# Kernel tuning notes

Measured on AMD Instinct MI355X. Metric: run time of the kernel, lower is better.

## Reference

```python
import jax, jax.numpy as jnp
import numpy as np

B, PD, CD = 8192, 1024, 1024


def setup_inputs() -> dict:
    key = jax.random.key(0)
    ks = jax.random.split(key, 10)
    u = lambda k, shape: jax.random.uniform(k, shape, dtype=jnp.float32, minval=-0.05, maxval=0.05)
    return {
        "P": jax.random.normal(ks[0], (B, PD), dtype=jnp.float32),
        "C1": jax.random.normal(ks[1], (B, CD), dtype=jnp.float32),
        "C2": jax.random.normal(ks[2], (B, CD), dtype=jnp.float32),
        "C3": jax.random.normal(ks[3], (B, CD), dtype=jnp.float32),
        "C4": jax.random.normal(ks[4], (B, CD), dtype=jnp.float32),
        "GateWeight_P": u(ks[5], (PD, CD)),
        "GateWeight_C": u(ks[6], (CD, CD)),
        "GateBias": u(ks[7], (CD,)),
        "OutWeight": u(ks[8], (PD, CD)),
        "OutBias": u(ks[9], (CD, 1)),
    }


def reference(P, C1, C2, C3, C4, GateWeight_P, GateWeight_C, GateBias, OutWeight, OutBias):
    # Stack the 4 choice branches: [4, B, C]
    Cs = jnp.stack([C1, C2, C3, C4], axis=0)
    WP = P @ GateWeight_P                                  # [B, C]
    WC = jnp.einsum("kbc,cd->kbd", Cs, GateWeight_C)       # [4, B, C]
    g = jax.nn.sigmoid(WP[None] + WC + GateBias)           # [4, B, C]
    C_dash = Cs * g                                        # [4, B, C]
    WP_out = P @ OutWeight                                 # [B, C]
    scores = jnp.einsum("kbc,bc->kb", C_dash, WP_out)      # batch_dot axes=[1,1]
    bias = jnp.einsum("kbc,c->kb", C_dash, OutBias[:, 0])  # K.dot(C_dash, OutBias)
    return (scores + bias).T                               # [B, 4]
```

## Files before the change

### kernel.cpp

```cpp
#include <hip/hip_runtime.h>
#include <hip/hip_bf16.h>


#define B_  8192
#define PD_ 1024
#define CD_ 1024

typedef unsigned short ushort_t;
typedef __attribute__((ext_vector_type(8))) short    short8;
typedef __attribute__((ext_vector_type(8))) unsigned short ushort8;
typedef __attribute__((ext_vector_type(4))) float    floatx4;

__device__ __forceinline__ float bf2f(unsigned short u) {
    return __uint_as_float(((unsigned)u) << 16);
}
__device__ __forceinline__ unsigned short f2bf(float f) {
    unsigned u = __float_as_uint(f);
    unsigned r = u + 0x7FFFu + ((u >> 16) & 1u);
    return (unsigned short)(r >> 16);
}

__global__ __launch_bounds__(256) void cast5_kernel(const float* __restrict__ P,
                                                    const float* __restrict__ C1,
                                                    const float* __restrict__ C2,
                                                    const float* __restrict__ C3,
                                                    const float* __restrict__ C4,
                                                    ushort_t* __restrict__ Pb,
                                                    ushort_t* __restrict__ Call) {
    const int seg = blockIdx.x >> 13;
    const int i   = (blockIdx.x & 8191) * 256 + threadIdx.x;
    const float* src;
    ushort_t* dst;
    switch (seg) {
        case 0: src = P;  dst = Pb; break;
        case 1: src = C1; dst = Call; break;
        case 2: src = C2; dst = Call + (size_t)1 * B_ * CD_; break;
        case 3: src = C3; dst = Call + (size_t)2 * B_ * CD_; break;
        default: src = C4; dst = Call + (size_t)3 * B_ * CD_; break;
    }
    float4 v = ((const float4*)src)[i];
    ushort4 o;
    o.x = f2bf(v.x); o.y = f2bf(v.y); o.z = f2bf(v.z); o.w = f2bf(v.w);
    ((ushort4*)dst)[i] = o;
}

__global__ __launch_bounds__(256) void transpose3(const float* __restrict__ GWP,
                                                  const float* __restrict__ OW,
                                                  const float* __restrict__ GWC,
                                                  ushort_t* __restrict__ Wcat,
                                                  ushort_t* __restrict__ GWCt) {
    __shared__ float tile[32][33];
    const float* src;
    ushort_t* dst;
    switch (blockIdx.z) {
        case 0: src = GWP; dst = Wcat; break;
        case 1: src = OW;  dst = Wcat + 1024 * 1024; break;
        default: src = GWC; dst = GWCt; break;
    }
    const int R = 1024, C = 1024;
    int c0 = blockIdx.x * 32, r0 = blockIdx.y * 32;
    int x = threadIdx.x, y = threadIdx.y;
    for (int i = y; i < 32; i += 8)
        tile[i][x] = src[(size_t)(r0 + i) * C + c0 + x];
    __syncthreads();
    for (int i = y; i < 32; i += 8)
        dst[(size_t)(c0 + i) * R + r0 + x] = f2bf(tile[x][i]);
}

__device__ __forceinline__ void gl_lds16(const void* g, void* l) {
    __builtin_amdgcn_global_load_lds((const __attribute__((address_space(1))) void*)g,
                                     (__attribute__((address_space(3))) void*)l, 16, 0, 0);
}

__global__ __launch_bounds__(256) void gemm_fused(const ushort_t* __restrict__ Pb,
                                                  const ushort_t* __restrict__ Wcat,
                                                  ushort_t* __restrict__ WPcat,
                                                  const ushort_t* __restrict__ Call,
                                                  const ushort_t* __restrict__ GWCt,
                                                  ushort_t* __restrict__ WC) {
    __shared__ ushort_t lA[128 * 32];
    __shared__ ushort_t lB[128 * 32];
    const int K = 1024;

    const ushort_t *A, *Bt;
    ushort_t* Cc;
    int N, tileM, tileN;
    const int bid = blockIdx.x;
    if (bid < 1024) {
        A = Pb; Bt = Wcat; Cc = WPcat; N = 2048;
        tileN = (bid & 15) * 128; tileM = (bid >> 4) * 128;
    } else {
        const int b2 = bid - 1024;
        A = Call; Bt = GWCt; Cc = WC; N = 1024;
        tileN = (b2 & 7) * 128; tileM = (b2 >> 3) * 128;
    }

    const int t    = threadIdx.x;
    const int wave = t >> 6, lane = t & 63;
    const int quad = lane >> 4, l16 = lane & 15;
    const int wm   = wave >> 1, wn  = wave & 1;

    const int ch0  = wave * 2;
    const int srow = lane >> 2;
    const int skc  = (lane & 3) ^ ((lane >> 4) & 3);
    const int sc   = skc * 8;
    const int lo0  = ch0 * 512 + lane * 8;

    const ushort_t* Ag0 = A  + (size_t)(tileM + ch0 * 16 + srow)      * K + sc;
    const ushort_t* Ag1 = A  + (size_t)(tileM + ch0 * 16 + srow + 16) * K + sc;
    const ushort_t* Bg0 = Bt + (size_t)(tileN + ch0 * 16 + srow)      * K + sc;
    const ushort_t* Bg1 = Bt + (size_t)(tileN + ch0 * 16 + srow + 16) * K + sc;

    const int fro = (l16 * 4 + (quad ^ (l16 >> 2))) * 8;

    floatx4 acc[4][4];
#pragma unroll
    for (int i = 0; i < 4; i++)
#pragma unroll
        for (int j = 0; j < 4; j++) acc[i][j] = (floatx4)0.f;

    for (int k0 = 0; k0 < K; k0 += 32) {
        gl_lds16(Ag0 + k0, &lA[lo0]);
        gl_lds16(Ag1 + k0, &lA[lo0 + 512]);
        gl_lds16(Bg0 + k0, &lB[lo0]);
        gl_lds16(Bg1 + k0, &lB[lo0 + 512]);
        __syncthreads();

        short8 af[4], bfr[4];
#pragma unroll
        for (int mi = 0; mi < 4; mi++)
            af[mi] = *(const short8*)&lA[(wm * 4 + mi) * 512 + fro];
#pragma unroll
        for (int ni = 0; ni < 4; ni++)
            bfr[ni] = *(const short8*)&lB[(wn * 4 + ni) * 512 + fro];
#pragma unroll
        for (int mi = 0; mi < 4; mi++)
#pragma unroll
            for (int ni = 0; ni < 4; ni++)
                acc[mi][ni] = __builtin_amdgcn_mfma_f32_16x16x32_bf16(
                    af[mi], bfr[ni], acc[mi][ni], 0, 0, 0);
        __syncthreads();
    }

#pragma unroll
    for (int mi = 0; mi < 4; mi++)
#pragma unroll
        for (int ni = 0; ni < 4; ni++)
#pragma unroll
            for (int r = 0; r < 4; r++) {
                int row = tileM + wm * 64 + mi * 16 + quad * 4 + r;
                int col = tileN + wn * 64 + ni * 16 + l16;
                Cc[(size_t)row * N + col] = f2bf(acc[mi][ni][r]);
            }
}

__global__ __launch_bounds__(256) void epilogue(const ushort_t* __restrict__ WPcat,
                                                const ushort_t* __restrict__ WC,
                                                const ushort_t* __restrict__ Call,
                                                const float* __restrict__ Gb,
                                                const float* __restrict__ Ob,
                                                float* __restrict__ out) {
    const int wave = threadIdx.x >> 6, lane = threadIdx.x & 63;
    const int b = blockIdx.x * 4 + wave;
    float acc[4] = {0.f, 0.f, 0.f, 0.f};

#pragma unroll
    for (int it = 0; it < 2; it++) {
        const int c = it * 512 + lane * 8;
        ushort8 wp  = *(const ushort8*)&WPcat[(size_t)b * 2048 + c];
        ushort8 wpo = *(const ushort8*)&WPcat[(size_t)b * 2048 + 1024 + c];
        floatx4 g0 = *(const floatx4*)&Gb[c];
        floatx4 g1 = *(const floatx4*)&Gb[c + 4];
        floatx4 o0 = *(const floatx4*)&Ob[c];
        floatx4 o1 = *(const floatx4*)&Ob[c + 4];
        float gb[8], ob[8];
#pragma unroll
        for (int j = 0; j < 4; j++) { gb[j] = g0[j]; gb[4 + j] = g1[j]; ob[j] = o0[j]; ob[4 + j] = o1[j]; }

        float po[8], wpf[8];
#pragma unroll
        for (int j = 0; j < 8; j++) {
            wpf[j] = bf2f(wp[j]);
            po[j]  = bf2f(wpo[j]) + ob[j];
        }
#pragma unroll
        for (int k = 0; k < 4; k++) {
            size_t off = ((size_t)k * B_ + b) * 1024 + c;
            ushort8 cv = *(const ushort8*)&Call[off];
            ushort8 wc = *(const ushort8*)&WC[off];
            float s = 0.f;
#pragma unroll
            for (int j = 0; j < 8; j++) {
                float x = wpf[j] + bf2f(wc[j]) + gb[j];
                float g = 1.f / (1.f + __expf(-x));
                s += bf2f(cv[j]) * g * po[j];
            }
            acc[k] += s;
        }
    }
#pragma unroll
    for (int k = 0; k < 4; k++) {
#pragma unroll
        for (int off = 32; off > 0; off >>= 1)
            acc[k] += __shfl_down(acc[k], off);
    }
    if (lane == 0) {
        out[(size_t)b * 4 + 0] = acc[0];
        out[(size_t)b * 4 + 1] = acc[1];
        out[(size_t)b * 4 + 2] = acc[2];
        out[(size_t)b * 4 + 3] = acc[3];
    }
}

extern "C" void kernel_launch(void* const* d_in, const int* in_sizes, int n_in,
                              void* d_out, int out_size, void* d_ws, size_t ws_size,
                              hipStream_t stream) {
    (void)in_sizes; (void)n_in; (void)out_size; (void)ws_size;
    const float* P   = (const float*)d_in[0];
    const float* C1  = (const float*)d_in[1];
    const float* C2  = (const float*)d_in[2];
    const float* C3  = (const float*)d_in[3];
    const float* C4  = (const float*)d_in[4];
    const float* GWP = (const float*)d_in[5];
    const float* GWC = (const float*)d_in[6];
    const float* Gb  = (const float*)d_in[7];
    const float* OW  = (const float*)d_in[8];
    const float* Ob  = (const float*)d_in[9];
    float* out = (float*)d_out;

    char* ws = (char*)d_ws;
    ushort_t* Pb    = (ushort_t*)(ws);
    ushort_t* Call  = (ushort_t*)(ws + (16u  << 20));
    ushort_t* Wcat  = (ushort_t*)(ws + (80u  << 20));
    ushort_t* GWCt  = (ushort_t*)(ws + (84u  << 20));
    ushort_t* WPcat = (ushort_t*)(ws + (86u  << 20));
    ushort_t* WC    = (ushort_t*)(ws + (118u << 20));

    cast5_kernel<<<5 * 8192, 256, 0, stream>>>(P, C1, C2, C3, C4, Pb, Call);
    transpose3<<<dim3(32, 32, 3), dim3(32, 8), 0, stream>>>(GWP, OW, GWC, Wcat, GWCt);

    gemm_fused<<<3072, 256, 0, stream>>>(Pb, Wcat, WPcat, Call, GWCt, WC);

    epilogue<<<B_ / 4, 256, 0, stream>>>(WPcat, WC, Call, Gb, Ob, out);
}
```

Baseline: 361.6 us.

## Fuse gating epilogue into choice GEMM with atomic score accumulation

The gate epilogue now runs inside the WC GEMM. Each block stages its bf16 WC tile in shared memory, computes the sigmoid gate and the dot-product contributions, and atomically adds partial scores to the output. This removes the write and re-read of the 64MB WC intermediate and one kernel launch. The cast and transpose prep kernels are merged into one launch that also zeroes the output. The P GEMM is split into its own kernel, which now runs before the choice GEMM instead of concurrently, and the fused epilogue adds atomics and scattered WPcat reads.

```diff
diff --git a/kernel.cpp b/kernel.cpp
--- a/kernel.cpp
+++ b/kernel.cpp
@@ -20,51 +20,60 @@
     return (unsigned short)(r >> 16);
 }
 
-__global__ __launch_bounds__(256) void cast5_kernel(const float* __restrict__ P,
-                                                    const float* __restrict__ C1,
-                                                    const float* __restrict__ C2,
-                                                    const float* __restrict__ C3,
-                                                    const float* __restrict__ C4,
-                                                    ushort_t* __restrict__ Pb,
-                                                    ushort_t* __restrict__ Call) {
-    const int seg = blockIdx.x >> 13;
-    const int i   = (blockIdx.x & 8191) * 256 + threadIdx.x;
-    const float* src;
-    ushort_t* dst;
-    switch (seg) {
-        case 0: src = P;  dst = Pb; break;
-        case 1: src = C1; dst = Call; break;
-        case 2: src = C2; dst = Call + (size_t)1 * B_ * CD_; break;
-        case 3: src = C3; dst = Call + (size_t)2 * B_ * CD_; break;
-        default: src = C4; dst = Call + (size_t)3 * B_ * CD_; break;
-    }
-    float4 v = ((const float4*)src)[i];
-    ushort4 o;
-    o.x = f2bf(v.x); o.y = f2bf(v.y); o.z = f2bf(v.z); o.w = f2bf(v.w);
-    ((ushort4*)dst)[i] = o;
-}
-
-__global__ __launch_bounds__(256) void transpose3(const float* __restrict__ GWP,
-                                                  const float* __restrict__ OW,
-                                                  const float* __restrict__ GWC,
-                                                  ushort_t* __restrict__ Wcat,
-                                                  ushort_t* __restrict__ GWCt) {
-    __shared__ float tile[32][33];
-    const float* src;
-    ushort_t* dst;
-    switch (blockIdx.z) {
-        case 0: src = GWP; dst = Wcat; break;
-        case 1: src = OW;  dst = Wcat + 1024 * 1024; break;
-        default: src = GWC; dst = GWCt; break;
-    }
-    const int R = 1024, C = 1024;
-    int c0 = blockIdx.x * 32, r0 = blockIdx.y * 32;
-    int x = threadIdx.x, y = threadIdx.y;
-    for (int i = y; i < 32; i += 8)
-        tile[i][x] = src[(size_t)(r0 + i) * C + c0 + x];
-    __syncthreads();
-    for (int i = y; i < 32; i += 8)
-        dst[(size_t)(c0 + i) * R + r0 + x] = f2bf(tile[x][i]);
+__global__ __launch_bounds__(256) void prep_kernel(const float* __restrict__ P,
+                                                   const float* __restrict__ C1,
+                                                   const float* __restrict__ C2,
+                                                   const float* __restrict__ C3,
+                                                   const float* __restrict__ C4,
+                                                   const float* __restrict__ GWP,
+                                                   const float* __restrict__ OW,
+                                                   const float* __restrict__ GWC,
+                                                   ushort_t* __restrict__ Pb,
+                                                   ushort_t* __restrict__ Call,
+                                                   ushort_t* __restrict__ Wcat,
+                                                   ushort_t* __restrict__ GWCt,
+                                                   float* __restrict__ out) {
+    const int bid = blockIdx.x;
+    const int tid = threadIdx.x;
+    if (bid < 40960) {
+        const int seg = bid >> 13;
+        const int i   = (bid & 8191) * 256 + tid;
+        const float* src;
+        ushort_t* dst;
+        switch (seg) {
+            case 0: src = P;  dst = Pb; break;
+            case 1: src = C1; dst = Call; break;
+            case 2: src = C2; dst = Call + (size_t)1 * B_ * CD_; break;
+            case 3: src = C3; dst = Call + (size_t)2 * B_ * CD_; break;
+            default: src = C4; dst = Call + (size_t)3 * B_ * CD_; break;
+        }
+        float4 v = ((const float4*)src)[i];
+        ushort4 o;
+        o.x = f2bf(v.x); o.y = f2bf(v.y); o.z = f2bf(v.z); o.w = f2bf(v.w);
+        ((ushort4*)dst)[i] = o;
+    } else if (bid < 44032) {
+        __shared__ float tile[32][33];
+        const int tb  = bid - 40960;
+        const int seg = tb >> 10;
+        const int t32 = tb & 1023;
+        const float* src;
+        ushort_t* dst;
+        switch (seg) {
+            case 0: src = GWP; dst = Wcat; break;
+            case 1: src = OW;  dst = Wcat + 1024 * 1024; break;
+            default: src = GWC; dst = GWCt; break;
+        }
+        const int c0 = (t32 & 31) * 32, r0 = (t32 >> 5) * 32;
+        const int x = tid & 31, y = tid >> 5;
+        for (int i = y; i < 32; i += 8)
+            tile[i][x] = src[(size_t)(r0 + i) * 1024 + c0 + x];
+        __syncthreads();
+        for (int i = y; i < 32; i += 8)
+            dst[(size_t)(c0 + i) * 1024 + r0 + x] = f2bf(tile[x][i]);
+    } else {
+        const int i = (bid - 44032) * 256 + tid;
+        ((float4*)out)[i] = float4{0.f, 0.f, 0.f, 0.f};
+    }
 }
 
 __device__ __forceinline__ void gl_lds16(const void* g, void* l) {
@@ -72,38 +81,22 @@
                                      (__attribute__((address_space(3))) void*)l, 16, 0, 0);
 }
 
-__global__ __launch_bounds__(256) void gemm_fused(const ushort_t* __restrict__ Pb,
-                                                  const ushort_t* __restrict__ Wcat,
-                                                  ushort_t* __restrict__ WPcat,
-                                                  const ushort_t* __restrict__ Call,
-                                                  const ushort_t* __restrict__ GWCt,
-                                                  ushort_t* __restrict__ WC) {
+__global__ __launch_bounds__(256) void gemmA(const ushort_t* __restrict__ A,
+                                             const ushort_t* __restrict__ Bt,
+                                             ushort_t* __restrict__ C) {
     __shared__ ushort_t lA[128 * 32];
     __shared__ ushort_t lB[128 * 32];
-    const int K = 1024;
-
-    const ushort_t *A, *Bt;
-    ushort_t* Cc;
-    int N, tileM, tileN;
-    const int bid = blockIdx.x;
-    if (bid < 1024) {
-        A = Pb; Bt = Wcat; Cc = WPcat; N = 2048;
-        tileN = (bid & 15) * 128; tileM = (bid >> 4) * 128;
-    } else {
-        const int b2 = bid - 1024;
-        A = Call; Bt = GWCt; Cc = WC; N = 1024;
-        tileN = (b2 & 7) * 128; tileM = (b2 >> 3) * 128;
-    }
-
-    const int t    = threadIdx.x;
+    const int K = 1024, N = 2048;
+    const int tileN = (blockIdx.x & 15) * 128, tileM = (blockIdx.x >> 4) * 128;
+
+    const int t = threadIdx.x;
     const int wave = t >> 6, lane = t & 63;
     const int quad = lane >> 4, l16 = lane & 15;
-    const int wm   = wave >> 1, wn  = wave & 1;
+    const int wm = wave >> 1, wn = wave & 1;
 
     const int ch0  = wave * 2;
     const int srow = lane >> 2;
-    const int skc  = (lane & 3) ^ ((lane >> 4) & 3);
-    const int sc   = skc * 8;
+    const int sc   = ((lane & 3) ^ ((lane >> 4) & 3)) * 8;
     const int lo0  = ch0 * 512 + lane * 8;
 
     const ushort_t* Ag0 = A  + (size_t)(tileM + ch0 * 16 + srow)      * K + sc;
@@ -125,7 +118,6 @@
         gl_lds16(Bg0 + k0, &lB[lo0]);
         gl_lds16(Bg1 + k0, &lB[lo0 + 512]);
         __syncthreads();
-
         short8 af[4], bfr[4];
 #pragma unroll
         for (int mi = 0; mi < 4; mi++)
@@ -141,7 +133,6 @@
                     af[mi], bfr[ni], acc[mi][ni], 0, 0, 0);
         __syncthreads();
     }
-
 #pragma unroll
     for (int mi = 0; mi < 4; mi++)
 #pragma unroll
@@ -150,66 +141,111 @@
             for (int r = 0; r < 4; r++) {
                 int row = tileM + wm * 64 + mi * 16 + quad * 4 + r;
                 int col = tileN + wn * 64 + ni * 16 + l16;
-                Cc[(size_t)row * N + col] = f2bf(acc[mi][ni][r]);
+                C[(size_t)row * N + col] = f2bf(acc[mi][ni][r]);
             }
 }
 
-__global__ __launch_bounds__(256) void epilogue(const ushort_t* __restrict__ WPcat,
-                                                const ushort_t* __restrict__ WC,
-                                                const ushort_t* __restrict__ Call,
-                                                const float* __restrict__ Gb,
-                                                const float* __restrict__ Ob,
-                                                float* __restrict__ out) {
-    const int wave = threadIdx.x >> 6, lane = threadIdx.x & 63;
-    const int b = blockIdx.x * 4 + wave;
-    float acc[4] = {0.f, 0.f, 0.f, 0.f};
-
-#pragma unroll
-    for (int it = 0; it < 2; it++) {
-        const int c = it * 512 + lane * 8;
-        ushort8 wp  = *(const ushort8*)&WPcat[(size_t)b * 2048 + c];
-        ushort8 wpo = *(const ushort8*)&WPcat[(size_t)b * 2048 + 1024 + c];
-        floatx4 g0 = *(const floatx4*)&Gb[c];
-        floatx4 g1 = *(const floatx4*)&Gb[c + 4];
-        floatx4 o0 = *(const floatx4*)&Ob[c];
-        floatx4 o1 = *(const floatx4*)&Ob[c + 4];
+__global__ __launch_bounds__(256) void gemmB_fused(const ushort_t* __restrict__ Call,
+                                                   const ushort_t* __restrict__ GWCt,
+                                                   const ushort_t* __restrict__ WPcat,
+                                                   const float* __restrict__ Gb,
+                                                   const float* __restrict__ Ob,
+                                                   float* __restrict__ out) {
+    __shared__ ushort_t smem[128 * 136];
+    ushort_t* lA = smem;
+    ushort_t* lB = smem + 4096;
+    const int K = 1024;
+    const int tileN = (blockIdx.x & 7) * 128, tileM = (blockIdx.x >> 3) * 128;
+
+    const int t = threadIdx.x;
+    const int wave = t >> 6, lane = t & 63;
+    const int quad = lane >> 4, l16 = lane & 15;
+    const int wm = wave >> 1, wn = wave & 1;
+
+    const int ch0  = wave * 2;
+    const int srow = lane >> 2;
+    const int sc   = ((lane & 3) ^ ((lane >> 4) & 3)) * 8;
+    const int lo0  = ch0 * 512 + lane * 8;
+
+    const ushort_t* Ag0 = Call + (size_t)(tileM + ch0 * 16 + srow)      * K + sc;
+    const ushort_t* Ag1 = Call + (size_t)(tileM + ch0 * 16 + srow + 16) * K + sc;
+    const ushort_t* Bg0 = GWCt + (size_t)(tileN + ch0 * 16 + srow)      * K + sc;
+    const ushort_t* Bg1 = GWCt + (size_t)(tileN + ch0 * 16 + srow + 16) * K + sc;
+
+    const int fro = (l16 * 4 + (quad ^ (l16 >> 2))) * 8;
+
+    floatx4 acc[4][4];
+#pragma unroll
+    for (int i = 0; i < 4; i++)
+#pragma unroll
+        for (int j = 0; j < 4; j++) acc[i][j] = (floatx4)0.f;
+
+    for (int k0 = 0; k0 < K; k0 += 32) {
+        gl_lds16(Ag0 + k0, &lA[lo0]);
+        gl_lds16(Ag1 + k0, &lA[lo0 + 512]);
+        gl_lds16(Bg0 + k0, &lB[lo0]);
+        gl_lds16(Bg1 + k0, &lB[lo0 + 512]);
+        __syncthreads();
+        short8 af[4], bfr[4];
+#pragma unroll
+        for (int mi = 0; mi < 4; mi++)
+            af[mi] = *(const short8*)&lA[(wm * 4 + mi) * 512 + fro];
+#pragma unroll
+        for (int ni = 0; ni < 4; ni++)
+            bfr[ni] = *(const short8*)&lB[(wn * 4 + ni) * 512 + fro];
+#pragma unroll
+        for (int mi = 0; mi < 4; mi++)
+#pragma unroll
+            for (int ni = 0; ni < 4; ni++)
+                acc[mi][ni] = __builtin_amdgcn_mfma_f32_16x16x32_bf16(
+                    af[mi], bfr[ni], acc[mi][ni], 0, 0, 0);
+        __syncthreads();
+    }
+
+#pragma unroll
+    for (int mi = 0; mi < 4; mi++)
+#pragma unroll
+        for (int ni = 0; ni < 4; ni++)
+#pragma unroll
+            for (int r = 0; r < 4; r++) {
+                int rl = wm * 64 + mi * 16 + quad * 4 + r;
+                int cl = wn * 64 + ni * 16 + l16;
+                smem[rl * 136 + cl] = f2bf(acc[mi][ni][r]);
+            }
+    __syncthreads();
+
+    const int rl   = t >> 1;
+    const int grow = tileM + rl;
+    const int kbr  = grow >> 13;
+    const int b    = grow & 8191;
+    const int ch   = (t & 1) * 64;
+
+    float s = 0.f;
+#pragma unroll
+    for (int j = 0; j < 8; j++) {
+        const int cl   = ch + j * 8;
+        const int gcol = tileN + cl;
+        ushort8 wc8  = *(const ushort8*)&smem[rl * 136 + cl];
+        ushort8 wp8  = *(const ushort8*)&WPcat[(size_t)b * 2048 + gcol];
+        ushort8 wpo8 = *(const ushort8*)&WPcat[(size_t)b * 2048 + 1024 + gcol];
+        ushort8 ck8  = *(const ushort8*)&Call[(size_t)grow * 1024 + gcol];
+        floatx4 g0 = *(const floatx4*)&Gb[gcol];
+        floatx4 g1 = *(const floatx4*)&Gb[gcol + 4];
+        floatx4 o0 = *(const floatx4*)&Ob[gcol];
+        floatx4 o1 = *(const floatx4*)&Ob[gcol + 4];
         float gb[8], ob[8];
 #pragma unroll
-        for (int j = 0; j < 4; j++) { gb[j] = g0[j]; gb[4 + j] = g1[j]; ob[j] = o0[j]; ob[4 + j] = o1[j]; }
-
-        float po[8], wpf[8];
-#pragma unroll
-        for (int j = 0; j < 8; j++) {
-            wpf[j] = bf2f(wp[j]);
-            po[j]  = bf2f(wpo[j]) + ob[j];
+        for (int q = 0; q < 4; q++) { gb[q] = g0[q]; gb[4 + q] = g1[q]; ob[q] = o0[q]; ob[4 + q] = o1[q]; }
+#pragma unroll
+        for (int q = 0; q < 8; q++) {
+            float x = bf2f(wp8[q]) + bf2f(wc8[q]) + gb[q];
+            float g = 1.f / (1.f + __expf(-x));
+            s += bf2f(ck8[q]) * g * (bf2f(wpo8[q]) + ob[q]);
         }
-#pragma unroll
-        for (int k = 0; k < 4; k++) {
-            size_t off = ((size_t)k * B_ + b) * 1024 + c;
-            ushort8 cv = *(const ushort8*)&Call[off];
-            ushort8 wc = *(const ushort8*)&WC[off];
-            float s = 0.f;
-#pragma unroll
-            for (int j = 0; j < 8; j++) {
-                float x = wpf[j] + bf2f(wc[j]) + gb[j];
-                float g = 1.f / (1.f + __expf(-x));
-                s += bf2f(cv[j]) * g * po[j];
-            }
-            acc[k] += s;
-        }
-    }
-#pragma unroll
-    for (int k = 0; k < 4; k++) {
-#pragma unroll
-        for (int off = 32; off > 0; off >>= 1)
-            acc[k] += __shfl_down(acc[k], off);
-    }
-    if (lane == 0) {
-        out[(size_t)b * 4 + 0] = acc[0];
-        out[(size_t)b * 4 + 1] = acc[1];
-        out[(size_t)b * 4 + 2] = acc[2];
-        out[(size_t)b * 4 + 3] = acc[3];
-    }
+    }
+    s += __shfl_xor(s, 1);
+    if ((t & 1) == 0)
+        atomicAdd(&out[(size_t)b * 4 + kbr], s);
 }
 
 extern "C" void kernel_launch(void* const* d_in, const int* in_sizes, int n_in,
@@ -230,16 +266,13 @@
 
     char* ws = (char*)d_ws;
     ushort_t* Pb    = (ushort_t*)(ws);
-    ushort_t* Call  = (ushort_t*)(ws + (16u  << 20));
-    ushort_t* Wcat  = (ushort_t*)(ws + (80u  << 20));
-    ushort_t* GWCt  = (ushort_t*)(ws + (84u  << 20));
-    ushort_t* WPcat = (ushort_t*)(ws + (86u  << 20));
-    ushort_t* WC    = (ushort_t*)(ws + (118u << 20));
-
-    cast5_kernel<<<5 * 8192, 256, 0, stream>>>(P, C1, C2, C3, C4, Pb, Call);
-    transpose3<<<dim3(32, 32, 3), dim3(32, 8), 0, stream>>>(GWP, OW, GWC, Wcat, GWCt);
-
-    gemm_fused<<<3072, 256, 0, stream>>>(Pb, Wcat, WPcat, Call, GWCt, WC);
-
-    epilogue<<<B_ / 4, 256, 0, stream>>>(WPcat, WC, Call, Gb, Ob, out);
-}
+    ushort_t* Call  = (ushort_t*)(ws + (16u << 20));
+    ushort_t* Wcat  = (ushort_t*)(ws + (80u << 20));
+    ushort_t* GWCt  = (ushort_t*)(ws + (84u << 20));
+    ushort_t* WPcat = (ushort_t*)(ws + (86u << 20));
+
+    prep_kernel<<<44064, 256, 0, stream>>>(P, C1, C2, C3, C4, GWP, OW, GWC,
+                                           Pb, Call, Wcat, GWCt, out);
+    gemmA<<<1024, 256, 0, stream>>>(Pb, Wcat, WPcat);
+    gemmB_fused<<<2048, 256, 0, stream>>>(Call, GWCt, WPcat, Gb, Ob, out);
+}
```

Measured after the change: 420.8 us. 1.16x slower.
